# Performance work log

Hardware: AMD Instinct MI355X
Metric: run time of the kernel (lower is better)

The kernel has to match this reference:

```python
import jax, jax.numpy as jnp
import numpy as np

ALPHA = 0.9
EPS = 1e-6


def setup_inputs() -> dict:
    key = jax.random.key(0)
    k1, k2 = jax.random.split(key)
    T, B, D, n = 4096, 16, 1024, 64
    x = jax.random.normal(k1, (T, B, D), dtype=jnp.float32)
    S = jnp.zeros((B, n, n), dtype=jnp.float32)
    # xavier-uniform-ish scale for each [n, D] block of the fused projection
    bound = np.sqrt(6.0 / (n + D))
    W_kvq = jax.random.uniform(k2, (3 * n, D), dtype=jnp.float32, minval=-bound, maxval=bound)
    return {"x": x, "S": S, "W_kvq": W_kvq}


def _e74_forward(x, S0, W_kvq):
    T, B, D = x.shape
    n = W_kvq.shape[0] // 3
    # fused k, v, q projection: [T, B, 3n]
    proj = jnp.einsum('tbd,nd->tbn', x, W_kvq)
    k_all, v_all, q_all = proj[..., :n], proj[..., n:2 * n], proj[..., 2 * n:]

    def step(S, kvq):
        k, v, q = kvq  # each [B, n]
        k_norm = k / (jnp.linalg.norm(k, axis=-1, keepdims=True) + EPS)
        retrieved = jnp.einsum('bij,bj->bi', S, k_norm)
        delta = v - retrieved
        S = ALPHA * S + delta[:, :, None] * k_norm[:, None, :]
        Sq = jnp.einsum('bij,bj->bi', S, q)
        out = Sq * jax.nn.silu(Sq)
        return S, out

    S_final, outputs = jax.lax.scan(step, S0, (k_all, v_all, q_all))
    return outputs, S_final  # [T, B, n], [B, n, n]


def reference(x, S, W_kvq):
    return _e74_forward(x, S, W_kvq)
```

## Files before the change

### kernel.cpp

```cpp
#include <hip/hip_runtime.h>

#define ALPHA 0.9f
#define EPS 1e-6f
#define LOG2A  (-0.15200309344504995f)
#define A64F   (1.1790184577738583e-3f)

constexpr int T_DIM  = 4096;
constexpr int B_DIM  = 16;
constexpr int D_DIM  = 1024;
constexpr int N_DIM  = 64;
constexpr int NPROJ  = 192;
constexpr int NCHUNK = 64;

typedef float  f32x4   __attribute__((ext_vector_type(4)));
typedef _Float16 f16x8 __attribute__((ext_vector_type(8)));

__device__ __forceinline__ float powA(float e) {
  return exp2f(e * LOG2A);
}
__device__ __forceinline__ float rdlane(float v, int src) {
  return __builtin_bit_cast(float,
      __builtin_amdgcn_readlane(__builtin_bit_cast(int, v), src));
}

__device__ __constant__ float APOW[16] = {
  1.f, 0.9f, 0.81f, 0.729f, 0.6561f, 0.59049f, 0.531441f, 0.4782969f,
  0.43046721f, 0.387420489f, 0.3486784401f, 0.31381059609f,
  0.282429536481f, 0.2541865828329f, 0.22876792454961f, 0.205891132094649f};
__device__ __constant__ float AINV[16] = {
  1.f, 1.1111111111f, 1.2345679012f, 1.3717421125f, 1.5241579028f,
  1.6935087809f, 1.8816764232f, 2.0907515814f, 2.3230573126f,
  2.5811747918f, 2.8679719909f, 3.1866355454f, 3.5407061616f,
  3.9341179573f, 4.3712421748f, 4.8569357498f};

__global__ __launch_bounds__(256) void convert_w(
    const float* __restrict__ W, _Float16* __restrict__ w16)
{
  int i = blockIdx.x * 256 + threadIdx.x;
  int c = i >> 10, k = i & 1023;
  w16[(k >> 5) * (NPROJ * 32) + c * 32 + (k & 31)] = (_Float16)W[i];
}

constexpr int BM = 128, BK = 32, NS = D_DIM / BK;

__global__ __launch_bounds__(512, 2) void proj_gemm(
    const float* __restrict__ x, const _Float16* __restrict__ w16,
    _Float16* __restrict__ pf16)
{
  __shared__ __align__(16) _Float16 smem[2 * BM * BK + 2 * NPROJ * BK];
  __shared__ float nrm[BM][2];

  _Float16 (*As)[BM * BK]    = (_Float16(*)[BM * BK])smem;
  _Float16 (*Bs)[NPROJ * BK] = (_Float16(*)[NPROJ * BK])(smem + 2 * BM * BK);
  _Float16 (*ep)[200]        = (_Float16(*)[200])smem;

  const int tid  = threadIdx.x;
  const int w    = tid >> 6, lane = tid & 63;
  const int wr   = w >> 2, wc = w & 3;
  const int fr   = lane & 15, fg = lane >> 4;
  const int row0 = blockIdx.x * BM;

  const int arow = tid >> 2, akq = (tid & 3) * 8;
  const float* aSrc = x + (size_t)(row0 + arow) * D_DIM + akq;

  f32x4 acc[4][3];
#pragma unroll
  for (int i = 0; i < 4; ++i)
#pragma unroll
    for (int j = 0; j < 3; ++j) acc[i][j] = (f32x4){0.f, 0.f, 0.f, 0.f};

  float4 a0, a1;

  auto loadA = [&](int s) {
    const float* p = aSrc + s * BK;
    a0 = *(const float4*)p;
    a1 = *(const float4*)(p + 4);
  };
  auto writeA = [&](int buf) {
    f16x8 h;
    h[0] = (_Float16)a0.x; h[1] = (_Float16)a0.y;
    h[2] = (_Float16)a0.z; h[3] = (_Float16)a0.w;
    h[4] = (_Float16)a1.x; h[5] = (_Float16)a1.y;
    h[6] = (_Float16)a1.z; h[7] = (_Float16)a1.w;
    *(f16x8*)&As[buf][arow * BK + akq] = h;
  };
  auto stageB = [&](int buf, int s) {
#pragma unroll
    for (int j = 0; j < 2; ++j) {
      const int sl = j * 8 + w;
      if (sl < 12) {
        const _Float16* src = w16 + (size_t)s * (NPROJ * 32) + sl * 512;
        __builtin_amdgcn_global_load_lds(
            (const __attribute__((address_space(1))) unsigned int*)(src) + lane * 4,
            (__attribute__((address_space(3))) unsigned int*)&Bs[buf][sl * 512],
            16, 0, 0);
      }
    }
  };
  auto compute = [&](int buf) {
    f16x8 af[4];
#pragma unroll
    for (int ar = 0; ar < 4; ++ar)
      af[ar] = *(const f16x8*)&As[buf][(wr * 64 + ar * 16 + fr) * BK + fg * 8];
#pragma unroll
    for (int bc = 0; bc < 3; ++bc) {
      f16x8 bf = *(const f16x8*)&Bs[buf][(wc * 48 + bc * 16 + fr) * BK + fg * 8];
#pragma unroll
      for (int ar = 0; ar < 4; ++ar)
        acc[ar][bc] = __builtin_amdgcn_mfma_f32_16x16x32_f16(af[ar], bf, acc[ar][bc], 0, 0, 0);
    }
  };

  loadA(0);
  stageB(0, 0);
  writeA(0);
  __syncthreads();

  int buf = 0;
  for (int s = 0; s < NS; ++s) {
    if (s + 1 < NS) {
      loadA(s + 1);
      stageB(buf ^ 1, s + 1);
    }
    compute(buf);
    if (s + 1 < NS) writeA(buf ^ 1);
    __syncthreads();
    buf ^= 1;
  }

  if (wc < 2) {
#pragma unroll
    for (int ar = 0; ar < 4; ++ar)
#pragma unroll
      for (int r = 0; r < 4; ++r) {
        float ss;
        if (wc == 0) {
          const float p0 = acc[ar][0][r], p1 = acc[ar][1][r], p2 = acc[ar][2][r];
          ss = p0 * p0 + p1 * p1 + p2 * p2;
        } else {
          const float p0 = acc[ar][0][r];
          ss = p0 * p0;
        }
        ss += __shfl_xor(ss, 1, 64);
        ss += __shfl_xor(ss, 2, 64);
        ss += __shfl_xor(ss, 4, 64);
        ss += __shfl_xor(ss, 8, 64);
        if (fr == 0) nrm[wr * 64 + ar * 16 + fg * 4 + r][wc] = ss;
      }
  }
  __syncthreads();
  if (wc < 2) {
#pragma unroll
    for (int ar = 0; ar < 4; ++ar)
#pragma unroll
      for (int r = 0; r < 4; ++r) {
        const int row = wr * 64 + ar * 16 + fg * 4 + r;
        const float rn = 1.0f / (sqrtf(nrm[row][0] + nrm[row][1]) + EPS);
        if (wc == 0) {
          acc[ar][0][r] *= rn; acc[ar][1][r] *= rn; acc[ar][2][r] *= rn;
        } else {
          acc[ar][0][r] *= rn;
        }
      }
  }

#pragma unroll
  for (int p = 0; p < 2; ++p) {
    __syncthreads();
    if (wr == p) {
#pragma unroll
      for (int ar = 0; ar < 4; ++ar)
#pragma unroll
        for (int bc = 0; bc < 3; ++bc)
#pragma unroll
          for (int r = 0; r < 4; ++r)
            ep[ar * 16 + fg * 4 + r][wc * 48 + bc * 16 + fr] = (_Float16)acc[ar][bc][r];
    }
    __syncthreads();
#pragma unroll
    for (int u = 0; u < 3; ++u) {
      const int g = u * 512 + tid;
      const int rr = g / 24, cc = g - rr * 24;
      *(f16x8*)(pf16 + (size_t)(row0 + p * 64 + rr) * NPROJ + cc * 8) =
          *(const f16x8*)&ep[rr][cc * 8];
    }
  }
}

__global__ __launch_bounds__(64) void scan_sw(
    const _Float16* __restrict__ pf16, const float* __restrict__ S0,
    float* __restrict__ out, float* __restrict__ Sfin)
{
  __shared__ __align__(16) _Float16 sK[64][72];
  __shared__ __align__(16) _Float16 sQ[32][72];
  __shared__ __align__(16) _Float16 sSW[64][72];
  __shared__ __align__(16) _Float16 sDT[64][72];
  __shared__ __align__(16) _Float16 sBB[16][72];
  __shared__ __align__(16) _Float16 uGt[16][72];

  const int lane = threadIdx.x;
  const int fr = lane & 15, fg = lane >> 4;
  const int b = blockIdx.x & (B_DIM - 1), c = blockIdx.x >> 4;
  const int t0o = c * 64;
  const bool c0 = (c == 0);

#pragma unroll
  for (int u = 0; u < 36; ++u) ((unsigned*)&sDT[0][0])[u * 64 + lane] = 0u;
#pragma unroll
  for (int u = 0; u < 9; ++u) ((unsigned*)&uGt[0][0])[u * 64 + lane] = 0u;

  auto stage64 = [&](_Float16 (*dst)[72], int t0, int sel) {
#pragma unroll
    for (int it = 0; it < 8; ++it) {
      int g = it * 64 + lane, t = g >> 3, c8 = g & 7;
      uint4 v = *(const uint4*)(pf16 + ((size_t)(t0 + t) * B_DIM + b) * NPROJ + sel + c8 * 8);
      *(uint4*)&dst[t][c8 * 8] = v;
    }
  };
  auto stageQ = [&](int half) {
#pragma unroll
    for (int it = 0; it < 4; ++it) {
      int g = it * 64 + lane, t = g >> 3, c8 = g & 7;
      uint4 v = *(const uint4*)(pf16 +
          ((size_t)(t0o + half * 32 + t) * B_DIM + b) * NPROJ + 128 + c8 * 8);
      *(uint4*)&sQ[t][c8 * 8] = v;
    }
  };

  auto dotT = [&](const _Float16* A, int sa, int ra, const _Float16* B, int sb, int rb) {
    f32x4 a = (f32x4){0.f, 0.f, 0.f, 0.f};
    f16x8 af = *(const f16x8*)(A + (ra + fr) * sa + fg * 8);
    f16x8 bf = *(const f16x8*)(B + (rb + fr) * sb + fg * 8);
    a = __builtin_amdgcn_mfma_f32_16x16x32_f16(af, bf, a, 0, 0, 0);
    af = *(const f16x8*)(A + (ra + fr) * sa + 32 + fg * 8);
    bf = *(const f16x8*)(B + (rb + fr) * sb + 32 + fg * 8);
    a = __builtin_amdgcn_mfma_f32_16x16x32_f16(af, bf, a, 0, 0, 0);
    return a;
  };

  auto transposeK = [&]() {
    f16x8 rv[8];
#pragma unroll
    for (int q8 = 0; q8 < 8; ++q8) rv[q8] = *(const f16x8*)&sK[lane][q8 * 8];
    asm volatile("" ::: "memory");
#pragma unroll
    for (int q8 = 0; q8 < 8; ++q8)
#pragma unroll
      for (int e = 0; e < 8; ++e) sK[q8 * 8 + e][lane] = rv[q8][e];
  };

  auto solve = [&](bool isW, int t0v) {
#pragma unroll
    for (int k = 0; k < 4; ++k) {
      _Float16 vr[16];
#pragma unroll
      for (int t = 0; t < 16; ++t)
        vr[t] = pf16[((size_t)(t0v + k * 16 + t) * B_DIM + b) * NPROJ + 64 + lane];

      if (k > 0) {
        f32x4 bacc[4];
#pragma unroll
        for (int ib = 0; ib < 4; ++ib) bacc[ib] = (f32x4){0.f, 0.f, 0.f, 0.f};
        for (int j = 0; j < k; ++j) {
          f32x4 g = dotT(&sK[0][0], 72, k * 16, &sK[0][0], 72, j * 16);
#pragma unroll
          for (int r = 0; r < 4; ++r) {
            const int tl = fg * 4 + r;
            const float e = isW ? (float)(16 * k + tl - 64)
                                : (float)(16 * (k - j) + tl - fr - 1);
            uGt[tl][fr] = (_Float16)(g[r] * powA(e));
          }
#pragma unroll
          for (int ib = 0; ib < 4; ++ib) {
            f16x8 af = *(const f16x8*)&uGt[fr][fg * 8];
            f16x8 bf = *(const f16x8*)&sDT[ib * 16 + fr][j * 16 + fg * 8];
            bacc[ib] = __builtin_amdgcn_mfma_f32_16x16x32_f16(af, bf, bacc[ib], 0, 0, 0);
          }
        }
#pragma unroll
        for (int ib = 0; ib < 4; ++ib)
#pragma unroll
          for (int r = 0; r < 4; ++r)
            sBB[fg * 4 + r][ib * 16 + fr] = (_Float16)bacc[ib][r];
      }

      const f32x4 gd = dotT(&sK[0][0], 72, k * 16, &sK[0][0], 72, k * 16);

      if (!isW) {
#pragma unroll
        for (int tj = 0; tj < 4; ++tj) {
          f32x4 a = dotT(&sK[0][0], 72, k * 16, &sSW[0][0], 72, tj * 16);
#pragma unroll
          for (int r = 0; r < 4; ++r)
            uGt[fg * 4 + r][tj * 16 + fr] =
                (_Float16)(a[r] * powA((float)(16 * k + fg * 4 + r)));
        }
      }

      float d[16], dA[16];
#pragma unroll
      for (int t = 0; t < 16; ++t) {
        float base = (float)vr[t];
        if (!isW) base -= (float)uGt[t][lane];
        if (k > 0) base -= (float)sBB[t][lane];
        float p0 = 0.f, p1 = 0.f, p2 = 0.f, p3 = 0.f;
#pragma unroll
        for (int tau = 0; tau < t; ++tau) {
          const float gv = rdlane(gd[t & 3], (t >> 2) * 16 + tau);
          if ((tau & 3) == 0)      p0 = fmaf(gv, dA[tau], p0);
          else if ((tau & 3) == 1) p1 = fmaf(gv, dA[tau], p1);
          else if ((tau & 3) == 2) p2 = fmaf(gv, dA[tau], p2);
          else                     p3 = fmaf(gv, dA[tau], p3);
        }
        const float sum = (p0 + p1) + (p2 + p3);
        d[t] = (t == 0) ? base : fmaf(-APOW[t - 1], sum, base);
        dA[t] = d[t] * AINV[t];
      }
#pragma unroll
      for (int t8 = 0; t8 < 2; ++t8) {
        f16x8 pack;
#pragma unroll
        for (int e = 0; e < 8; ++e) {
          const int tl = t8 * 8 + e;
          const float sc = isW ? powA((float)(63 - (16 * k + tl))) : 1.f;
          pack[e] = (_Float16)(d[tl] * sc);
        }
        *(f16x8*)&sDT[lane][k * 16 + t8 * 8] = pack;
      }

      if (!isW) {
#pragma unroll
        for (int u = 0; u < 2; ++u) {
          const int idx = lane * 2 + u;
          *((unsigned*)&uGt[idx >> 3][16] + (idx & 7)) = 0u;
        }
      }
    }
  };

  if (!c0) {
    stage64(sK, t0o - 64, 0);
    solve(true, t0o - 64);
    transposeK();
#pragma unroll
    for (int ti = 0; ti < 4; ++ti)
#pragma unroll
      for (int tj = 0; tj < 4; ++tj) {
        f32x4 a = dotT(&sDT[0][0], 72, ti * 16, &sK[0][0], 72, tj * 16);
#pragma unroll
        for (int r = 0; r < 4; ++r)
          sSW[ti * 16 + fg * 4 + r][tj * 16 + fr] = (_Float16)a[r];
      }
  } else {
#pragma unroll
    for (int it = 0; it < 8; ++it) {
      const int row = it * 8 + (lane >> 3), col = (lane & 7) * 8;
      const float* src = S0 + (size_t)b * 4096 + row * 64 + col;
      const float4 v1 = *(const float4*)src;
      const float4 v2 = *(const float4*)(src + 4);
      f16x8 pk;
      pk[0] = (_Float16)v1.x; pk[1] = (_Float16)v1.y;
      pk[2] = (_Float16)v1.z; pk[3] = (_Float16)v1.w;
      pk[4] = (_Float16)v2.x; pk[5] = (_Float16)v2.y;
      pk[6] = (_Float16)v2.z; pk[7] = (_Float16)v2.w;
      *(f16x8*)&sSW[row][col] = pk;
    }
  }

  stage64(sK, t0o, 0);
  stageQ(0);
  solve(false, t0o);

#pragma unroll
  for (int h2 = 0; h2 < 2; ++h2) {
    if (h2) stageQ(1);
#pragma unroll
    for (int tb2 = 0; tb2 < 2; ++tb2) {
      const int tb = h2 * 2 + tb2;
      f32x4 sq[4];
#pragma unroll
      for (int tj = 0; tj < 4; ++tj) {
        f32x4 a = dotT(&sQ[0][0], 72, tb2 * 16, &sSW[0][0], 72, tj * 16);
#pragma unroll
        for (int r = 0; r < 4; ++r)
          a[r] *= powA((float)(tb * 16 + fg * 4 + r + 1));
        sq[tj] = a;
      }
      for (int qb = 0; qb <= tb; ++qb) {
        f32x4 h = dotT(&sQ[0][0], 72, tb2 * 16, &sK[0][0], 72, qb * 16);
#pragma unroll
        for (int r = 0; r < 4; ++r) {
          const int tl = fg * 4 + r;
          const int t = tb * 16 + tl, tau = qb * 16 + fr;
          const float val = (tau <= t) ? h[r] * powA((float)(t - tau)) : 0.f;
          uGt[tl][fr] = (_Float16)val;
        }
#pragma unroll
        for (int ib = 0; ib < 4; ++ib) {
          f16x8 af = *(const f16x8*)&uGt[fr][fg * 8];
          f16x8 bf = *(const f16x8*)&sDT[ib * 16 + fr][qb * 16 + fg * 8];
          sq[ib] = __builtin_amdgcn_mfma_f32_16x16x32_f16(af, bf, sq[ib], 0, 0, 0);
        }
      }
#pragma unroll
      for (int tj = 0; tj < 4; ++tj)
#pragma unroll
        for (int r = 0; r < 4; ++r) {
          const int t = tb * 16 + fg * 4 + r, i = tj * 16 + fr;
          const float Sq = sq[tj][r];
          const float sig = 1.0f / (1.0f + __expf(-Sq));
          out[(size_t)(t0o + t) * 1024 + b * 64 + i] = Sq * Sq * sig;
        }
    }
  }

  if (c == NCHUNK - 1) {
#pragma unroll
    for (int t8 = 0; t8 < 8; ++t8) {
      f16x8 v = *(const f16x8*)&sDT[lane][t8 * 8];
#pragma unroll
      for (int e = 0; e < 8; ++e)
        v[e] = (_Float16)((float)v[e] * powA((float)(63 - (t8 * 8 + e))));
      *(f16x8*)&sDT[lane][t8 * 8] = v;
    }
    transposeK();
#pragma unroll
    for (int ti = 0; ti < 4; ++ti)
#pragma unroll
      for (int tj = 0; tj < 4; ++tj) {
        f32x4 so = dotT(&sDT[0][0], 72, ti * 16, &sK[0][0], 72, tj * 16);
#pragma unroll
        for (int r = 0; r < 4; ++r) {
          const int i = ti * 16 + fg * 4 + r, j = tj * 16 + fr;
          Sfin[((size_t)b * 64 + i) * 64 + j] = A64F * (float)sSW[i][j] + so[r];
        }
      }
  }
}

extern "C" void kernel_launch(void* const* d_in, const int* in_sizes, int n_in,
                              void* d_out, int out_size, void* d_ws, size_t ws_size,
                              hipStream_t stream)
{
  const float* x  = (const float*)d_in[0];
  const float* S0 = (const float*)d_in[1];
  const float* Wk = (const float*)d_in[2];
  float* out  = (float*)d_out;
  float* Sfin = out + (size_t)T_DIM * B_DIM * N_DIM;

  char* wsb = (char*)d_ws;
  _Float16* pf16 = (_Float16*)(wsb);
  _Float16* w16  = (_Float16*)(wsb + 25165824);

  convert_w<<<(NPROJ * D_DIM) / 256, 256, 0, stream>>>(Wk, w16);
  proj_gemm<<<(T_DIM * B_DIM) / BM, 512, 0, stream>>>(x, w16, pf16);
  scan_sw<<<B_DIM * NCHUNK, 64, 0, stream>>>(pf16, S0, out, Sfin);
}
```

Baseline: 106.0 us.

## Deepen GEMM prefetch, double-buffer uGt, fold S*K term into MFMA accumulator

```diff
diff --git a/kernel.cpp b/kernel.cpp
--- a/kernel.cpp
+++ b/kernel.cpp
@@ -114,16 +114,17 @@
   loadA(0);
   stageB(0, 0);
   writeA(0);
+  loadA(1);
   __syncthreads();
 
   int buf = 0;
   for (int s = 0; s < NS; ++s) {
     if (s + 1 < NS) {
-      loadA(s + 1);
       stageB(buf ^ 1, s + 1);
+      writeA(buf ^ 1);
+      if (s + 2 < NS) loadA(s + 2);
     }
     compute(buf);
-    if (s + 1 < NS) writeA(buf ^ 1);
     __syncthreads();
     buf ^= 1;
   }
@@ -196,7 +197,7 @@
   __shared__ __align__(16) _Float16 sSW[64][72];
   __shared__ __align__(16) _Float16 sDT[64][72];
   __shared__ __align__(16) _Float16 sBB[16][72];
-  __shared__ __align__(16) _Float16 uGt[16][72];
+  __shared__ __align__(16) _Float16 uGt[2][16][40];
 
   const int lane = threadIdx.x;
   const int fr = lane & 15, fg = lane >> 4;
@@ -207,7 +208,7 @@
 #pragma unroll
   for (int u = 0; u < 36; ++u) ((unsigned*)&sDT[0][0])[u * 64 + lane] = 0u;
 #pragma unroll
-  for (int u = 0; u < 9; ++u) ((unsigned*)&uGt[0][0])[u * 64 + lane] = 0u;
+  for (int u = 0; u < 10; ++u) ((unsigned*)&uGt[0][0][0])[u * 64 + lane] = 0u;
 
   auto stage64 = [&](_Float16 (*dst)[72], int t0, int sel) {
 #pragma unroll
@@ -250,6 +251,11 @@
   };
 
   auto solve = [&](bool isW, int t0v) {
+    f32x4 gdA[4];
+#pragma unroll
+    for (int k = 0; k < 4; ++k)
+      gdA[k] = dotT(&sK[0][0], 72, k * 16, &sK[0][0], 72, k * 16);
+
 #pragma unroll
     for (int k = 0; k < 4; ++k) {
       _Float16 vr[16];
@@ -257,10 +263,11 @@
       for (int t = 0; t < 16; ++t)
         vr[t] = pf16[((size_t)(t0v + k * 16 + t) * B_DIM + b) * NPROJ + 64 + lane];
 
+      f32x4 bacc[4];
+#pragma unroll
+      for (int ib = 0; ib < 4; ++ib) bacc[ib] = (f32x4){0.f, 0.f, 0.f, 0.f};
+
       if (k > 0) {
-        f32x4 bacc[4];
-#pragma unroll
-        for (int ib = 0; ib < 4; ++ib) bacc[ib] = (f32x4){0.f, 0.f, 0.f, 0.f};
         for (int j = 0; j < k; ++j) {
           f32x4 g = dotT(&sK[0][0], 72, k * 16, &sK[0][0], 72, j * 16);
 #pragma unroll
@@ -268,15 +275,29 @@
             const int tl = fg * 4 + r;
             const float e = isW ? (float)(16 * k + tl - 64)
                                 : (float)(16 * (k - j) + tl - fr - 1);
-            uGt[tl][fr] = (_Float16)(g[r] * powA(e));
+            uGt[j & 1][tl][fr] = (_Float16)(g[r] * powA(e));
           }
 #pragma unroll
           for (int ib = 0; ib < 4; ++ib) {
-            f16x8 af = *(const f16x8*)&uGt[fr][fg * 8];
+            f16x8 af = *(const f16x8*)&uGt[j & 1][fr][fg * 8];
             f16x8 bf = *(const f16x8*)&sDT[ib * 16 + fr][j * 16 + fg * 8];
             bacc[ib] = __builtin_amdgcn_mfma_f32_16x16x32_f16(af, bf, bacc[ib], 0, 0, 0);
           }
         }
+      }
+
+      if (!isW) {
+#pragma unroll
+        for (int tj = 0; tj < 4; ++tj) {
+          f32x4 a = dotT(&sK[0][0], 72, k * 16, &sSW[0][0], 72, tj * 16);
+#pragma unroll
+          for (int r = 0; r < 4; ++r)
+            bacc[tj][r] = fmaf(a[r], powA((float)(16 * k + fg * 4 + r)), bacc[tj][r]);
+        }
+      }
+
+      const bool useBB = (!isW || k > 0);
+      if (useBB) {
 #pragma unroll
         for (int ib = 0; ib < 4; ++ib)
 #pragma unroll
@@ -284,25 +305,13 @@
             sBB[fg * 4 + r][ib * 16 + fr] = (_Float16)bacc[ib][r];
       }
 
-      const f32x4 gd = dotT(&sK[0][0], 72, k * 16, &sK[0][0], 72, k * 16);
-
-      if (!isW) {
-#pragma unroll
-        for (int tj = 0; tj < 4; ++tj) {
-          f32x4 a = dotT(&sK[0][0], 72, k * 16, &sSW[0][0], 72, tj * 16);
-#pragma unroll
-          for (int r = 0; r < 4; ++r)
-            uGt[fg * 4 + r][tj * 16 + fr] =
-                (_Float16)(a[r] * powA((float)(16 * k + fg * 4 + r)));
-        }
-      }
+      const f32x4 gd = gdA[k];
 
       float d[16], dA[16];
 #pragma unroll
       for (int t = 0; t < 16; ++t) {
         float base = (float)vr[t];
-        if (!isW) base -= (float)uGt[t][lane];
-        if (k > 0) base -= (float)sBB[t][lane];
+        if (useBB) base -= (float)sBB[t][lane];
         float p0 = 0.f, p1 = 0.f, p2 = 0.f, p3 = 0.f;
 #pragma unroll
         for (int tau = 0; tau < t; ++tau) {
@@ -326,14 +335,6 @@
           pack[e] = (_Float16)(d[tl] * sc);
         }
         *(f16x8*)&sDT[lane][k * 16 + t8 * 8] = pack;
-      }
-
-      if (!isW) {
-#pragma unroll
-        for (int u = 0; u < 2; ++u) {
-          const int idx = lane * 2 + u;
-          *((unsigned*)&uGt[idx >> 3][16] + (idx & 7)) = 0u;
-        }
       }
     }
   };
@@ -393,11 +394,11 @@
           const int tl = fg * 4 + r;
           const int t = tb * 16 + tl, tau = qb * 16 + fr;
           const float val = (tau <= t) ? h[r] * powA((float)(t - tau)) : 0.f;
-          uGt[tl][fr] = (_Float16)val;
+          uGt[qb & 1][tl][fr] = (_Float16)val;
         }
 #pragma unroll
         for (int ib = 0; ib < 4; ++ib) {
-          f16x8 af = *(const f16x8*)&uGt[fr][fg * 8];
+          f16x8 af = *(const f16x8*)&uGt[qb & 1][fr][fg * 8];
           f16x8 bf = *(const f16x8*)&sDT[ib * 16 + fr][qb * 16 + fg * 8];
           sq[ib] = __builtin_amdgcn_mfma_f32_16x16x32_f16(af, bf, sq[ib], 0, 0, 0);
         }
```

Result: no change. 107.5 us (+1.4%).
